# Kernel optimization log

Measured on AMD Instinct MI355X. Metric: run time of the kernel, lower is better.

Reference implementation:

```python
import jax, jax.numpy as jnp
import numpy as np
from jax import lax


def _conv(x, w, b):
    # x: [B,C,H,W] NCHW, w: [O,I,3,3] OIHW, SAME padding, stride 1
    y = lax.conv_general_dilated(x, w, (1, 1), 'SAME',
                                 dimension_numbers=('NCHW', 'OIHW', 'NCHW'))
    return y + b[None, :, None, None]


def _maxpool2(x):
    return lax.reduce_window(x, -jnp.inf, lax.max,
                             (1, 1, 2, 2), (1, 1, 2, 2), 'VALID')


def _squash(x):
    # x: [..., D]
    norm = jnp.sum(x * x, axis=-1, keepdims=True)
    scale = norm / (1.0 + norm) / jnp.sqrt(norm + 1e-9)
    return scale * x


def _routing(x, W):
    # x: [B, R, C]  (R routes, C in_channels); W: [N, R, C, O]
    # u_hat[b,n,r,o] = sum_c x[b,r,c] * W[n,r,c,o]
    u_hat = jnp.einsum('brc,nrco->bnro', x, W)
    B, N, R, O = u_hat.shape
    b_ij = jnp.zeros((B, N, R), dtype=u_hat.dtype)
    v = None
    for it in range(3):  # fixed 3 routing iterations
        c_ij = jax.nn.softmax(b_ij, axis=2)
        s_j = jnp.einsum('bnr,bnro->bno', c_ij, u_hat)
        v = _squash(s_j)
        if it < 2:
            b_ij = b_ij + jnp.einsum('bnro,bno->bnr', u_hat, v)
    return v  # [B, N, O]


def setup_inputs() -> dict:
    key = jax.random.key(0)
    ks = jax.random.split(key, 10)
    B = 512
    num_classes = 15
    x = jax.random.normal(ks[0], (B, 3, 64, 64), dtype=jnp.float32)

    def kaiming(k, shape, fan_in):
        return jax.random.normal(k, shape, dtype=jnp.float32) * np.sqrt(2.0 / fan_in)

    w1 = kaiming(ks[1], (8, 3, 3, 3), 3 * 9)
    b1 = jnp.zeros((8,), jnp.float32)
    w2 = kaiming(ks[2], (16, 8, 3, 3), 8 * 9)
    b2 = jnp.zeros((16,), jnp.float32)
    w3 = kaiming(ks[3], (32, 16, 3, 3), 16 * 9)
    b3 = jnp.zeros((32,), jnp.float32)
    # route_weights are torch.randn in the original (std 1.0)
    rw1 = jax.random.normal(ks[4], (32, 64, 32, 8), dtype=jnp.float32)   # primary
    rw2 = jax.random.normal(ks[5], (num_classes, 32, 8, 16), dtype=jnp.float32)  # secondary
    fc_w = kaiming(ks[6], (num_classes, 16 * num_classes), 16 * num_classes)
    fc_b = jnp.zeros((num_classes,), jnp.float32)
    return {'x': x, 'w1': w1, 'b1': b1, 'w2': w2, 'b2': b2,
            'w3': w3, 'b3': b3, 'rw1': rw1, 'rw2': rw2,
            'fc_w': fc_w, 'fc_b': fc_b}


def reference(x, w1, b1, w2, b2, w3, b3, rw1, rw2, fc_w, fc_b):
    h = _maxpool2(jax.nn.relu(_conv(x, w1, b1)))   # [B,8,32,32]
    h = _maxpool2(jax.nn.relu(_conv(h, w2, b2)))   # [B,16,16,16]
    h = _maxpool2(jax.nn.relu(_conv(h, w3, b3)))   # [B,32,8,8]
    B = h.shape[0]
    # routes = 64 spatial positions, channels = 32 capsule input features
    feats = h.reshape(B, 32, 64).transpose(0, 2, 1)  # [B, 64, 32]
    v1 = _routing(feats, rw1)   # [B, 32, 8]
    v2 = _routing(v1, rw2)      # [B, 15, 16]
    flat = v2.reshape(B, -1)    # [B, 240]
    return flat @ fc_w.T + fc_b  # [B, 15]
```

## Files before the change

kernel.cpp:

```cpp
#include <hip/hip_runtime.h>
#include <hip/hip_bf16.h>


template<int CIN, int COUT, int HIN, int NO>
__global__ __launch_bounds__(256)
void conv_relu_pool(const float* __restrict__ in, const float* __restrict__ w,
                    const float* __restrict__ bias, float* __restrict__ out)
{
    constexpr int HOUT = HIN / 2;
    constexpr int PR = HIN + 2;
    constexpr int PC = (HIN + 2 + 3) & ~3;
    constexpr int NS = HIN / 8;
    constexpr int NOP = COUT / NO;
    constexpr int NTASK = NOP * HOUT * NS;
    constexpr int XWORDS = CIN * PR * PC;
    constexpr int WWORDS = CIN * 9 * COUT;

    __shared__ float xin[CIN][PR][PC];
    __shared__ float wt[WWORDS];
    __shared__ float bl[COUT];

    const int tid = threadIdx.x;
    const int b   = blockIdx.x;

    for (int i = tid; i < XWORDS; i += 256) ((float*)xin)[i] = 0.f;
    for (int i = tid; i < WWORDS; i += 256) {
        int o = i % COUT, k = (i / COUT) % 9, c = i / (COUT * 9);
        wt[i] = w[(o * CIN + c) * 9 + k];
    }
    if (tid < COUT) bl[tid] = bias[tid];
    __syncthreads();

    const float4* gin = (const float4*)(in + (size_t)b * CIN * HIN * HIN);
    constexpr int CHUNKS = CIN * HIN * (HIN / 4);
    for (int i = tid; i < CHUNKS; i += 256) {
        float4 v = gin[i];
        int ch = i % (HIN / 4);
        int y  = (i / (HIN / 4)) % HIN;
        int c  = i / ((HIN / 4) * HIN);
        float* dst = &xin[c][y + 1][ch * 4 + 1];
        dst[0] = v.x; dst[1] = v.y; dst[2] = v.z; dst[3] = v.w;
    }
    __syncthreads();

    for (int task = tid; task < NTASK; task += 256) {
        const int s  = task % NS;
        const int py = (task / NS) % HOUT;
        const int o0 = (task / (NS * HOUT)) * NO;
        const int X0 = s * 8;

        float acc[NO][2][8];
#pragma unroll
        for (int n = 0; n < NO; ++n)
#pragma unroll
            for (int q = 0; q < 2; ++q)
#pragma unroll
                for (int j = 0; j < 8; ++j) acc[n][q][j] = 0.f;

        for (int c = 0; c < CIN; ++c) {
            float rows[4][12];
#pragma unroll
            for (int rr = 0; rr < 4; ++rr) {
                const float4* src = (const float4*)&xin[c][2 * py + rr][X0];
#pragma unroll
                for (int j = 0; j < 3; ++j) {
                    float4 v = src[j];
                    rows[rr][j * 4 + 0] = v.x; rows[rr][j * 4 + 1] = v.y;
                    rows[rr][j * 4 + 2] = v.z; rows[rr][j * 4 + 3] = v.w;
                }
            }
            const float* wc = wt + c * 9 * COUT;
#pragma unroll
            for (int ky = 0; ky < 3; ++ky) {
#pragma unroll
                for (int n = 0; n < NO; ++n) {
                    const float w0 = wc[(ky * 3 + 0) * COUT + o0 + n];
                    const float w1 = wc[(ky * 3 + 1) * COUT + o0 + n];
                    const float w2 = wc[(ky * 3 + 2) * COUT + o0 + n];
#pragma unroll
                    for (int j = 0; j < 8; ++j) {
                        acc[n][0][j] = fmaf(rows[ky][j],     w0, acc[n][0][j]);
                        acc[n][0][j] = fmaf(rows[ky][j + 1], w1, acc[n][0][j]);
                        acc[n][0][j] = fmaf(rows[ky][j + 2], w2, acc[n][0][j]);
                        acc[n][1][j] = fmaf(rows[ky + 1][j],     w0, acc[n][1][j]);
                        acc[n][1][j] = fmaf(rows[ky + 1][j + 1], w1, acc[n][1][j]);
                        acc[n][1][j] = fmaf(rows[ky + 1][j + 2], w2, acc[n][1][j]);
                    }
                }
            }
        }
#pragma unroll
        for (int n = 0; n < NO; ++n) {
            const float bv = bl[o0 + n];
            float4 ov;
            float* p = (float*)&ov;
#pragma unroll
            for (int j = 0; j < 4; ++j) {
                float m = fmaxf(fmaxf(acc[n][0][2 * j], acc[n][0][2 * j + 1]),
                                fmaxf(acc[n][1][2 * j], acc[n][1][2 * j + 1]));
                p[j] = fmaxf(m + bv, 0.f);
            }
            float* po = out + (((size_t)b * COUT + o0 + n) * HOUT + py) * HOUT + s * 4;
            *(float4*)po = ov;
        }
    }
}

__global__ __launch_bounds__(256)
void transpose_w1(const float* __restrict__ W, float* __restrict__ Wt)
{
    int idx = blockIdx.x * 256 + threadIdx.x;
    if (idx >= 32 * 32 * 64 * 2) return;
    int half = idx & 1;
    int r    = (idx >> 1) & 63;
    int c    = (idx >> 7) & 31;
    int n    = idx >> 12;
    ((float4*)Wt)[idx] =
        ((const float4*)W)[(((n * 64 + r) * 32 + c) << 1) + half];
}

__global__ __launch_bounds__(256)
void routing1_reg(const float* __restrict__ h3, const float* __restrict__ Wt,
                  float* __restrict__ v1)
{
    constexpr int C = 32, R = 64, O = 8, G = 8;
    const int lane = threadIdx.x & 63;
    const int n    = blockIdx.y * 4 + (threadIdx.x >> 6);
    const int b0   = blockIdx.x * G;

    float u[G][O];
#pragma unroll
    for (int g = 0; g < G; ++g)
#pragma unroll
        for (int o = 0; o < O; ++o) u[g][o] = 0.f;

    const float4* wp = (const float4*)Wt + (size_t)n * C * R * 2;
    const float* xb = h3 + (size_t)b0 * (C * R) + lane;

#pragma unroll 2
    for (int c = 0; c < C; ++c) {
        float xv[G];
#pragma unroll
        for (int g = 0; g < G; ++g) xv[g] = xb[(size_t)g * (C * R) + c * R];
        float4 w0 = wp[(c * R + lane) * 2];
        float4 w1 = wp[(c * R + lane) * 2 + 1];
#pragma unroll
        for (int g = 0; g < G; ++g) {
            u[g][0] = fmaf(xv[g], w0.x, u[g][0]);
            u[g][1] = fmaf(xv[g], w0.y, u[g][1]);
            u[g][2] = fmaf(xv[g], w0.z, u[g][2]);
            u[g][3] = fmaf(xv[g], w0.w, u[g][3]);
            u[g][4] = fmaf(xv[g], w1.x, u[g][4]);
            u[g][5] = fmaf(xv[g], w1.y, u[g][5]);
            u[g][6] = fmaf(xv[g], w1.z, u[g][6]);
            u[g][7] = fmaf(xv[g], w1.w, u[g][7]);
        }
    }

    float bij[G];
#pragma unroll
    for (int g = 0; g < G; ++g) bij[g] = 0.f;
    float s[G][O];

    for (int it = 0; it < 3; ++it) {
        float cc[G];
#pragma unroll
        for (int g = 0; g < G; ++g) {
            float mx = bij[g];
#pragma unroll
            for (int w = 1; w < 64; w <<= 1) mx = fmaxf(mx, __shfl_xor(mx, w, 64));
            float e = __expf(bij[g] - mx);
            float sum = e;
#pragma unroll
            for (int w = 1; w < 64; w <<= 1) sum += __shfl_xor(sum, w, 64);
            cc[g] = e / sum;
        }
#pragma unroll
        for (int g = 0; g < G; ++g)
#pragma unroll
            for (int o = 0; o < O; ++o) s[g][o] = cc[g] * u[g][o];
#pragma unroll
        for (int w = 1; w < 64; w <<= 1)
#pragma unroll
            for (int g = 0; g < G; ++g)
#pragma unroll
                for (int o = 0; o < O; ++o) s[g][o] += __shfl_xor(s[g][o], w, 64);
#pragma unroll
        for (int g = 0; g < G; ++g) {
            float nr = 0.f;
#pragma unroll
            for (int o = 0; o < O; ++o) nr = fmaf(s[g][o], s[g][o], nr);
            float scale = nr / (1.f + nr) / sqrtf(nr + 1e-9f);
#pragma unroll
            for (int o = 0; o < O; ++o) s[g][o] *= scale;
            if (it < 2) {
                float d = 0.f;
#pragma unroll
                for (int o = 0; o < O; ++o) d = fmaf(u[g][o], s[g][o], d);
                bij[g] += d;
            }
        }
    }
    float outv = 0.f;
#pragma unroll
    for (int g = 0; g < G; ++g)
#pragma unroll
        for (int o = 0; o < O; ++o)
            outv = (lane == g * O + o) ? s[g][o] : outv;
    v1[(size_t)(b0 + (lane >> 3)) * 256 + n * 8 + (lane & 7)] = outv;
}

__global__ __launch_bounds__(256)
void routing2_fc(const float* __restrict__ v1, const float* __restrict__ W,
                 const float* __restrict__ fcw, const float* __restrict__ fcb,
                 float* __restrict__ out)
{
    constexpr int R = 32, C = 8, O = 16;
    __shared__ float vv[240];

    const int t  = threadIdx.x;
    const int b  = blockIdx.x;
    const int wv = t >> 6;
    const int lane = t & 63;
    const int nh = lane >> 5;
    const int r  = lane & 31;

    const float4* xr = (const float4*)(v1 + (size_t)b * 256 + r * 8);
    float4 x0 = xr[0], x1 = xr[1];
    float xv[8] = {x0.x, x0.y, x0.z, x0.w, x1.x, x1.y, x1.z, x1.w};

    float u[2][O];
    int nn[2];
#pragma unroll
    for (int p = 0; p < 2; ++p) {
        int n = wv * 4 + p * 2 + nh;
        nn[p] = n;
        int ncl = n < 15 ? n : 14;
        const float4* wp = (const float4*)(W + ((size_t)(ncl * R + r) * C) * O);
#pragma unroll
        for (int o = 0; o < O; ++o) u[p][o] = 0.f;
#pragma unroll
        for (int c = 0; c < C; ++c) {
#pragma unroll
            for (int j = 0; j < 4; ++j) {
                float4 w4 = wp[c * 4 + j];
                u[p][j * 4 + 0] = fmaf(xv[c], w4.x, u[p][j * 4 + 0]);
                u[p][j * 4 + 1] = fmaf(xv[c], w4.y, u[p][j * 4 + 1]);
                u[p][j * 4 + 2] = fmaf(xv[c], w4.z, u[p][j * 4 + 2]);
                u[p][j * 4 + 3] = fmaf(xv[c], w4.w, u[p][j * 4 + 3]);
            }
        }
    }

    float bij[2] = {0.f, 0.f};
    float s[2][O];
    for (int it = 0; it < 3; ++it) {
#pragma unroll
        for (int p = 0; p < 2; ++p) {
            float mx = bij[p];
#pragma unroll
            for (int w = 1; w < 32; w <<= 1) mx = fmaxf(mx, __shfl_xor(mx, w, 32));
            float e = __expf(bij[p] - mx);
            float sum = e;
#pragma unroll
            for (int w = 1; w < 32; w <<= 1) sum += __shfl_xor(sum, w, 32);
            float cc = e / sum;
#pragma unroll
            for (int o = 0; o < O; ++o) s[p][o] = cc * u[p][o];
        }
#pragma unroll
        for (int w = 1; w < 32; w <<= 1)
#pragma unroll
            for (int p = 0; p < 2; ++p)
#pragma unroll
                for (int o = 0; o < O; ++o) s[p][o] += __shfl_xor(s[p][o], w, 32);
#pragma unroll
        for (int p = 0; p < 2; ++p) {
            float nr = 0.f;
#pragma unroll
            for (int o = 0; o < O; ++o) nr = fmaf(s[p][o], s[p][o], nr);
            float scale = nr / (1.f + nr) / sqrtf(nr + 1e-9f);
#pragma unroll
            for (int o = 0; o < O; ++o) s[p][o] *= scale;
            if (it < 2) {
                float d = 0.f;
#pragma unroll
                for (int o = 0; o < O; ++o) d = fmaf(u[p][o], s[p][o], d);
                bij[p] += d;
            }
        }
    }
#pragma unroll
    for (int p = 0; p < 2; ++p) {
        float outv = 0.f;
#pragma unroll
        for (int o = 0; o < O; ++o) outv = (r == o) ? s[p][o] : outv;
        if (r < O && nn[p] < 15) vv[nn[p] * O + r] = outv;
    }
    __syncthreads();
    if (t < 240) {
        int j = t >> 4, k0 = t & 15;
        float acc = 0.f;
        for (int k = k0; k < 240; k += 16) acc = fmaf(vv[k], fcw[j * 240 + k], acc);
#pragma unroll
        for (int w = 1; w < 16; w <<= 1) acc += __shfl_xor(acc, w, 16);
        if (k0 == 0) out[(size_t)b * 15 + j] = acc + fcb[j];
    }
}

extern "C" void kernel_launch(void* const* d_in, const int* in_sizes, int n_in,
                              void* d_out, int out_size, void* d_ws, size_t ws_size,
                              hipStream_t stream) {
    const float* x    = (const float*)d_in[0];
    const float* w1   = (const float*)d_in[1];
    const float* b1   = (const float*)d_in[2];
    const float* w2   = (const float*)d_in[3];
    const float* b2   = (const float*)d_in[4];
    const float* w3   = (const float*)d_in[5];
    const float* b3   = (const float*)d_in[6];
    const float* rw1  = (const float*)d_in[7];
    const float* rw2  = (const float*)d_in[8];
    const float* fcw  = (const float*)d_in[9];
    const float* fcb  = (const float*)d_in[10];
    float* out = (float*)d_out;

    const int B = 512;
    float* ws = (float*)d_ws;
    float* h1 = ws;
    float* h2 = h1 + (size_t)B * 8 * 32 * 32;
    float* h3 = h2 + (size_t)B * 16 * 16 * 16;
    float* v1 = h3 + (size_t)B * 32 * 8 * 8;
    float* Wt = h2;

    conv_relu_pool<3, 8, 64, 4><<<B, 256, 0, stream>>>(x, w1, b1, h1);
    conv_relu_pool<8, 16, 32, 4><<<B, 256, 0, stream>>>(h1, w2, b2, h2);
    conv_relu_pool<16, 32, 16, 2><<<B, 256, 0, stream>>>(h2, w3, b3, h3);
    transpose_w1<<<(32 * 32 * 64 * 2 + 255) / 256, 256, 0, stream>>>(rw1, Wt);
    {
        dim3 grid(B / 8, 8);
        routing1_reg<<<grid, 256, 0, stream>>>(h3, Wt, v1);
    }
    routing2_fc<<<B, 256, 0, stream>>>(v1, rw2, fcw, fcb, out);
}
```

Baseline: 232.5 us.

## Split conv into row bands and replace routing shuffle reductions with halving transposes

The conv kernels now split each image into row bands across a second grid dimension, with one task per thread, so more blocks run and each stages a smaller padded input tile in LDS. Both routing kernels swap the full per-element butterfly shuffle reductions for a recursive-halving reduce that leaves each lane holding one output element. Small LDS scratch plus lgkmcnt waits broadcast the reduced values. Routing1 also halves the batch group per block to cut register pressure, at the cost of reloading weights for more blocks. The LDS exchange relies on s_waitcnt without a barrier, which only holds within a single wavefront.

```diff
diff --git a/kernel.cpp b/kernel.cpp
--- a/kernel.cpp
+++ b/kernel.cpp
@@ -2,26 +2,67 @@
 #include <hip/hip_bf16.h>
 
 
-template<int CIN, int COUT, int HIN, int NO>
+__device__ __forceinline__ void lds_fence() {
+    asm volatile("s_waitcnt lgkmcnt(0)" ::: "memory");
+}
+
+template<int NV>
+__device__ __forceinline__ float halve_sum(float* t, int lane) {
+#pragma unroll
+    for (int m = NV >> 1; m >= 1; m >>= 1) {
+        bool hi = (lane & m) != 0;
+#pragma unroll
+        for (int j = 0; j < m; ++j) {
+            float keep = hi ? t[j + m] : t[j];
+            float send = hi ? t[j] : t[j + m];
+            t[j] = keep + __shfl_xor(send, m, 64);
+        }
+    }
+    float v = t[0];
+#pragma unroll
+    for (int m = NV; m < 64; m <<= 1) v += __shfl_xor(v, m, 64);
+    return v;
+}
+
+template<int NV>
+__device__ __forceinline__ float halve_max(float* t, int lane) {
+#pragma unroll
+    for (int m = NV >> 1; m >= 1; m >>= 1) {
+        bool hi = (lane & m) != 0;
+#pragma unroll
+        for (int j = 0; j < m; ++j) {
+            float keep = hi ? t[j + m] : t[j];
+            float send = hi ? t[j] : t[j + m];
+            t[j] = fmaxf(keep, __shfl_xor(send, m, 64));
+        }
+    }
+    float v = t[0];
+#pragma unroll
+    for (int m = NV; m < 64; m <<= 1) v = fmaxf(v, __shfl_xor(v, m, 64));
+    return v;
+}
+
+template<int CIN, int COUT, int HIN, int NO, int BANDH>
 __global__ __launch_bounds__(256)
 void conv_relu_pool(const float* __restrict__ in, const float* __restrict__ w,
                     const float* __restrict__ bias, float* __restrict__ out)
 {
     constexpr int HOUT = HIN / 2;
-    constexpr int PR = HIN + 2;
+    constexpr int ROWS = 2 * BANDH + 2;
     constexpr int PC = (HIN + 2 + 3) & ~3;
     constexpr int NS = HIN / 8;
-    constexpr int NOP = COUT / NO;
-    constexpr int NTASK = NOP * HOUT * NS;
-    constexpr int XWORDS = CIN * PR * PC;
+    constexpr int XWORDS = CIN * ROWS * PC;
     constexpr int WWORDS = CIN * 9 * COUT;
-
-    __shared__ float xin[CIN][PR][PC];
+    static_assert((COUT / NO) * BANDH * NS == 256, "one task per thread");
+
+    __shared__ float xin[CIN][ROWS][PC];
     __shared__ float wt[WWORDS];
     __shared__ float bl[COUT];
 
-    const int tid = threadIdx.x;
-    const int b   = blockIdx.x;
+    const int tid  = threadIdx.x;
+    const int b    = blockIdx.x;
+    const int band = blockIdx.y;
+    const int y0   = 2 * (band * BANDH) - 1;
 
     for (int i = tid; i < XWORDS; i += 256) ((float*)xin)[i] = 0.f;
     for (int i = tid; i < WWORDS; i += 256) {
@@ -32,77 +73,78 @@
     __syncthreads();
 
     const float4* gin = (const float4*)(in + (size_t)b * CIN * HIN * HIN);
-    constexpr int CHUNKS = CIN * HIN * (HIN / 4);
+    constexpr int CHUNKS = CIN * ROWS * (HIN / 4);
     for (int i = tid; i < CHUNKS; i += 256) {
-        float4 v = gin[i];
         int ch = i % (HIN / 4);
-        int y  = (i / (HIN / 4)) % HIN;
-        int c  = i / ((HIN / 4) * HIN);
-        float* dst = &xin[c][y + 1][ch * 4 + 1];
-        dst[0] = v.x; dst[1] = v.y; dst[2] = v.z; dst[3] = v.w;
+        int ly = (i / (HIN / 4)) % ROWS;
+        int c  = i / ((HIN / 4) * ROWS);
+        int y  = y0 + ly;
+        if (y >= 0 && y < HIN) {
+            float4 v = gin[(c * HIN + y) * (HIN / 4) + ch];
+            float* dst = &xin[c][ly][1 + ch * 4];
+            dst[0] = v.x; dst[1] = v.y; dst[2] = v.z; dst[3] = v.w;
+        }
     }
     __syncthreads();
 
-    for (int task = tid; task < NTASK; task += 256) {
-        const int s  = task % NS;
-        const int py = (task / NS) % HOUT;
-        const int o0 = (task / (NS * HOUT)) * NO;
-        const int X0 = s * 8;
-
-        float acc[NO][2][8];
-#pragma unroll
-        for (int n = 0; n < NO; ++n)
-#pragma unroll
-            for (int q = 0; q < 2; ++q)
-#pragma unroll
-                for (int j = 0; j < 8; ++j) acc[n][q][j] = 0.f;
-
-        for (int c = 0; c < CIN; ++c) {
-            float rows[4][12];
-#pragma unroll
-            for (int rr = 0; rr < 4; ++rr) {
-                const float4* src = (const float4*)&xin[c][2 * py + rr][X0];
-#pragma unroll
-                for (int j = 0; j < 3; ++j) {
-                    float4 v = src[j];
-                    rows[rr][j * 4 + 0] = v.x; rows[rr][j * 4 + 1] = v.y;
-                    rows[rr][j * 4 + 2] = v.z; rows[rr][j * 4 + 3] = v.w;
+    const int s  = tid % NS;
+    const int py = (tid / NS) % BANDH;
+    const int o0 = (tid / (NS * BANDH)) * NO;
+    const int X0 = s * 8;
+
+    float acc[NO][2][8];
+#pragma unroll
+    for (int n = 0; n < NO; ++n)
+#pragma unroll
+        for (int q = 0; q < 2; ++q)
+#pragma unroll
+            for (int j = 0; j < 8; ++j) acc[n][q][j] = 0.f;
+
+    for (int c = 0; c < CIN; ++c) {
+        float rows[4][12];
+#pragma unroll
+        for (int rr = 0; rr < 4; ++rr) {
+            const float4* src = (const float4*)&xin[c][2 * py + rr][X0];
+#pragma unroll
+            for (int j = 0; j < 3; ++j) {
+                float4 v = src[j];
+                rows[rr][j * 4 + 0] = v.x; rows[rr][j * 4 + 1] = v.y;
+                rows[rr][j * 4 + 2] = v.z; rows[rr][j * 4 + 3] = v.w;
+            }
+        }
+        const float* wc = wt + c * 9 * COUT;
+#pragma unroll
+        for (int ky = 0; ky < 3; ++ky) {
+#pragma unroll
+            for (int n = 0; n < NO; ++n) {
+                const float w0 = wc[(ky * 3 + 0) * COUT + o0 + n];
+                const float w1 = wc[(ky * 3 + 1) * COUT + o0 + n];
+                const float w2 = wc[(ky * 3 + 2) * COUT + o0 + n];
+#pragma unroll
+                for (int j = 0; j < 8; ++j) {
+                    acc[n][0][j] = fmaf(rows[ky][j],     w0, acc[n][0][j]);
+                    acc[n][0][j] = fmaf(rows[ky][j + 1], w1, acc[n][0][j]);
+                    acc[n][0][j] = fmaf(rows[ky][j + 2], w2, acc[n][0][j]);
+                    acc[n][1][j] = fmaf(rows[ky + 1][j],     w0, acc[n][1][j]);
+                    acc[n][1][j] = fmaf(rows[ky + 1][j + 1], w1, acc[n][1][j]);
+                    acc[n][1][j] = fmaf(rows[ky + 1][j + 2], w2, acc[n][1][j]);
                 }
             }
-            const float* wc = wt + c * 9 * COUT;
-#pragma unroll
-            for (int ky = 0; ky < 3; ++ky) {
-#pragma unroll
-                for (int n = 0; n < NO; ++n) {
-                    const float w0 = wc[(ky * 3 + 0) * COUT + o0 + n];
-                    const float w1 = wc[(ky * 3 + 1) * COUT + o0 + n];
-                    const float w2 = wc[(ky * 3 + 2) * COUT + o0 + n];
-#pragma unroll
-                    for (int j = 0; j < 8; ++j) {
-                        acc[n][0][j] = fmaf(rows[ky][j],     w0, acc[n][0][j]);
-                        acc[n][0][j] = fmaf(rows[ky][j + 1], w1, acc[n][0][j]);
-                        acc[n][0][j] = fmaf(rows[ky][j + 2], w2, acc[n][0][j]);
-                        acc[n][1][j] = fmaf(rows[ky + 1][j],     w0, acc[n][1][j]);
-                        acc[n][1][j] = fmaf(rows[ky + 1][j + 1], w1, acc[n][1][j]);
-                        acc[n][1][j] = fmaf(rows[ky + 1][j + 2], w2, acc[n][1][j]);
-                    }
-                }
-            }
-        }
-#pragma unroll
-        for (int n = 0; n < NO; ++n) {
-            const float bv = bl[o0 + n];
-            float4 ov;
-            float* p = (float*)&ov;
-#pragma unroll
-            for (int j = 0; j < 4; ++j) {
-                float m = fmaxf(fmaxf(acc[n][0][2 * j], acc[n][0][2 * j + 1]),
-                                fmaxf(acc[n][1][2 * j], acc[n][1][2 * j + 1]));
-                p[j] = fmaxf(m + bv, 0.f);
-            }
-            float* po = out + (((size_t)b * COUT + o0 + n) * HOUT + py) * HOUT + s * 4;
-            *(float4*)po = ov;
-        }
+        }
+    }
+#pragma unroll
+    for (int n = 0; n < NO; ++n) {
+        const float bv = bl[o0 + n];
+        float4 ov;
+        float* p = (float*)&ov;
+#pragma unroll
+        for (int j = 0; j < 4; ++j) {
+            float m = fmaxf(fmaxf(acc[n][0][2 * j], acc[n][0][2 * j + 1]),
+                            fmaxf(acc[n][1][2 * j], acc[n][1][2 * j + 1]));
+            p[j] = fmaxf(m + bv, 0.f);
+        }
+        float* po = out + (((size_t)b * COUT + o0 + n) * HOUT + band * BANDH + py) * HOUT + s * 4;
+        *(float4*)po = ov;
     }
 }
 
@@ -123,9 +165,12 @@
 void routing1_reg(const float* __restrict__ h3, const float* __restrict__ Wt,
                   float* __restrict__ v1)
 {
-    constexpr int C = 32, R = 64, O = 8, G = 8;
+    constexpr int C = 32, R = 64, O = 8, G = 4;
+    __shared__ float sh[4][48];
+
     const int lane = threadIdx.x & 63;
-    const int n    = blockIdx.y * 4 + (threadIdx.x >> 6);
+    const int wv   = threadIdx.x >> 6;
+    const int n    = blockIdx.y * 4 + wv;
     const int b0   = blockIdx.x * G;
 
     float u[G][O];
@@ -137,7 +182,7 @@
     const float4* wp = (const float4*)Wt + (size_t)n * C * R * 2;
     const float* xb = h3 + (size_t)b0 * (C * R) + lane;
 
-#pragma unroll 2
+#pragma unroll 4
     for (int c = 0; c < C; ++c) {
         float xv[G];
 #pragma unroll
@@ -157,57 +202,66 @@
         }
     }
 
-    float bij[G];
-#pragma unroll
-    for (int g = 0; g < G; ++g) bij[g] = 0.f;
-    float s[G][O];
+    float bij[G] = {0.f, 0.f, 0.f, 0.f};
+    float v_own = 0.f;
 
     for (int it = 0; it < 3; ++it) {
+        float t4[G];
+#pragma unroll
+        for (int g = 0; g < G; ++g) t4[g] = bij[g];
+        float mred = halve_max<G>(t4, lane);
+        if (lane < G) sh[wv][lane] = mred;
+        lds_fence();
+        float4 mx4 = *(const float4*)&sh[wv][0];
+        const float* mxp = (const float*)&mx4;
+        float e[G];
+#pragma unroll
+        for (int g = 0; g < G; ++g) {
+            e[g] = __expf(bij[g] - mxp[g]);
+            t4[g] = e[g];
+        }
+        float sred = halve_sum<G>(t4, lane);
+        if (lane < G) sh[wv][4 + lane] = sred;
+        lds_fence();
+        float4 sm4 = *(const float4*)&sh[wv][4];
+        const float* smp = (const float*)&sm4;
         float cc[G];
 #pragma unroll
-        for (int g = 0; g < G; ++g) {
-            float mx = bij[g];
-#pragma unroll
-            for (int w = 1; w < 64; w <<= 1) mx = fmaxf(mx, __shfl_xor(mx, w, 64));
-            float e = __expf(bij[g] - mx);
-            float sum = e;
-#pragma unroll
-            for (int w = 1; w < 64; w <<= 1) sum += __shfl_xor(sum, w, 64);
-            cc[g] = e / sum;
-        }
+        for (int g = 0; g < G; ++g) cc[g] = e[g] / smp[g];
+
+        float t32[G * O];
 #pragma unroll
         for (int g = 0; g < G; ++g)
 #pragma unroll
-            for (int o = 0; o < O; ++o) s[g][o] = cc[g] * u[g][o];
-#pragma unroll
-        for (int w = 1; w < 64; w <<= 1)
-#pragma unroll
-            for (int g = 0; g < G; ++g)
-#pragma unroll
-                for (int o = 0; o < O; ++o) s[g][o] += __shfl_xor(s[g][o], w, 64);
-#pragma unroll
-        for (int g = 0; g < G; ++g) {
-            float nr = 0.f;
-#pragma unroll
-            for (int o = 0; o < O; ++o) nr = fmaf(s[g][o], s[g][o], nr);
-            float scale = nr / (1.f + nr) / sqrtf(nr + 1e-9f);
-#pragma unroll
-            for (int o = 0; o < O; ++o) s[g][o] *= scale;
-            if (it < 2) {
+            for (int o = 0; o < O; ++o) t32[g * O + o] = cc[g] * u[g][o];
+        float s_own = halve_sum<G * O>(t32, lane);
+
+        float nr = s_own * s_own;
+#pragma unroll
+        for (int m = 1; m < O; m <<= 1) nr += __shfl_xor(nr, m, 64);
+        float scale = nr / (1.f + nr) / sqrtf(nr + 1e-9f);
+        v_own = s_own * scale;
+
+        if (it < 2) {
+            if (lane < G * O) sh[wv][8 + lane] = v_own;
+            lds_fence();
+            const float4* vr4 = (const float4*)&sh[wv][8];
+#pragma unroll
+            for (int g = 0; g < G; ++g) {
+                float4 a = vr4[g * 2], bq = vr4[g * 2 + 1];
                 float d = 0.f;
-#pragma unroll
-                for (int o = 0; o < O; ++o) d = fmaf(u[g][o], s[g][o], d);
+                d = fmaf(u[g][0], a.x, d);  d = fmaf(u[g][1], a.y, d);
+                d = fmaf(u[g][2], a.z, d);  d = fmaf(u[g][3], a.w, d);
+                d = fmaf(u[g][4], bq.x, d); d = fmaf(u[g][5], bq.y, d);
+                d = fmaf(u[g][6], bq.z, d); d = fmaf(u[g][7], bq.w, d);
                 bij[g] += d;
             }
         }
     }
-    float outv = 0.f;
-#pragma unroll
-    for (int g = 0; g < G; ++g)
-#pragma unroll
-        for (int o = 0; o < O; ++o)
-            outv = (lane == g * O + o) ? s[g][o] : outv;
-    v1[(size_t)(b0 + (lane >> 3)) * 256 + n * 8 + (lane & 7)] = outv;
+    if (lane < G * O) {
+        int g = lane >> 3, o = lane & 7;
+        v1[(size_t)(b0 + g) * 256 + n * 8 + o] = v_own;
+    }
 }
 
 __global__ __launch_bounds__(256)
@@ -217,6 +271,7 @@
 {
     constexpr int R = 32, C = 8, O = 16;
     __shared__ float vv[240];
+    __shared__ float sh2[4][64];
 
     const int t  = threadIdx.x;
     const int b  = blockIdx.x;
@@ -253,49 +308,70 @@
     }
 
     float bij[2] = {0.f, 0.f};
-    float s[2][O];
+    float v_own = 0.f;
+    const int po = r >> 4;
+    const int oo = r & 15;
+
     for (int it = 0; it < 3; ++it) {
+        float cc[2];
 #pragma unroll
         for (int p = 0; p < 2; ++p) {
             float mx = bij[p];
 #pragma unroll
-            for (int w = 1; w < 32; w <<= 1) mx = fmaxf(mx, __shfl_xor(mx, w, 32));
+            for (int w = 1; w < 32; w <<= 1) mx = fmaxf(mx, __shfl_xor(mx, w, 64));
             float e = __expf(bij[p] - mx);
             float sum = e;
 #pragma unroll
-            for (int w = 1; w < 32; w <<= 1) sum += __shfl_xor(sum, w, 32);
-            float cc = e / sum;
-#pragma unroll
-            for (int o = 0; o < O; ++o) s[p][o] = cc * u[p][o];
-        }
-#pragma unroll
-        for (int w = 1; w < 32; w <<= 1)
-#pragma unroll
-            for (int p = 0; p < 2; ++p)
-#pragma unroll
-                for (int o = 0; o < O; ++o) s[p][o] += __shfl_xor(s[p][o], w, 32);
-#pragma unroll
-        for (int p = 0; p < 2; ++p) {
-            float nr = 0.f;
-#pragma unroll
-            for (int o = 0; o < O; ++o) nr = fmaf(s[p][o], s[p][o], nr);
-            float scale = nr / (1.f + nr) / sqrtf(nr + 1e-9f);
-#pragma unroll
-            for (int o = 0; o < O; ++o) s[p][o] *= scale;
-            if (it < 2) {
+            for (int w = 1; w < 32; w <<= 1) sum += __shfl_xor(sum, w, 64);
+            cc[p] = e / sum;
+        }
+        float t32[32];
+#pragma unroll
+        for (int p = 0; p < 2; ++p)
+#pragma unroll
+            for (int o = 0; o < O; ++o) t32[p * O + o] = cc[p] * u[p][o];
+        float s_own;
+        {
+#pragma unroll
+            for (int m = 16; m >= 1; m >>= 1) {
+                bool hi = (r & m) != 0;
+#pragma unroll
+                for (int j = 0; j < m; ++j) {
+                    float keep = hi ? t32[j + m] : t32[j];
+                    float send = hi ? t32[j] : t32[j + m];
+                    t32[j] = keep + __shfl_xor(send, m, 64);
+                }
+            }
+            s_own = t32[0];
+        }
+        float nr = s_own * s_own;
+#pragma unroll
+        for (int m = 1; m < O; m <<= 1) nr += __shfl_xor(nr, m, 64);
+        float scale = nr / (1.f + nr) / sqrtf(nr + 1e-9f);
+        v_own = s_own * scale;
+
+        if (it < 2) {
+            sh2[wv][lane] = v_own;
+            lds_fence();
+            const float4* vr4 = (const float4*)&sh2[wv][nh * 32];
+#pragma unroll
+            for (int p = 0; p < 2; ++p) {
                 float d = 0.f;
 #pragma unroll
-                for (int o = 0; o < O; ++o) d = fmaf(u[p][o], s[p][o], d);
+                for (int j = 0; j < 4; ++j) {
+                    float4 a = vr4[p * 4 + j];
+                    d = fmaf(u[p][j * 4 + 0], a.x, d);
+                    d = fmaf(u[p][j * 4 + 1], a.y, d);
+                    d = fmaf(u[p][j * 4 + 2], a.z, d);
+                    d = fmaf(u[p][j * 4 + 3], a.w, d);
+                }
                 bij[p] += d;
             }
         }
     }
-#pragma unroll
-    for (int p = 0; p < 2; ++p) {
-        float outv = 0.f;
-#pragma unroll
-        for (int o = 0; o < O; ++o) outv = (r == o) ? s[p][o] : outv;
-        if (r < O && nn[p] < 15) vv[nn[p] * O + r] = outv;
+    {
+        int n = wv * 4 + po * 2 + nh;
+        if (n < 15) vv[n * O + oo] = v_own;
     }
     __syncthreads();
     if (t < 240) {
@@ -332,12 +408,12 @@
     float* v1 = h3 + (size_t)B * 32 * 8 * 8;
     float* Wt = h2;
 
-    conv_relu_pool<3, 8, 64, 4><<<B, 256, 0, stream>>>(x, w1, b1, h1);
-    conv_relu_pool<8, 16, 32, 4><<<B, 256, 0, stream>>>(h1, w2, b2, h2);
-    conv_relu_pool<16, 32, 16, 2><<<B, 256, 0, stream>>>(h2, w3, b3, h3);
+    conv_relu_pool<3, 8, 64, 2, 8><<<dim3(B, 4), 256, 0, stream>>>(x, w1, b1, h1);
+    conv_relu_pool<8, 16, 32, 2, 8><<<dim3(B, 2), 256, 0, stream>>>(h1, w2, b2, h2);
+    conv_relu_pool<16, 32, 16, 2, 8><<<dim3(B, 1), 256, 0, stream>>>(h2, w3, b3, h3);
     transpose_w1<<<(32 * 32 * 64 * 2 + 255) / 256, 256, 0, stream>>>(rw1, Wt);
     {
-        dim3 grid(B / 8, 8);
+        dim3 grid(B / 4, 8);
         routing1_reg<<<grid, 256, 0, stream>>>(h3, Wt, v1);
     }
     routing2_fc<<<B, 256, 0, stream>>>(v1, rw2, fcw, fcb, out);
```

Measured after the change: 388.0 us. +66.9%, slower.
